# Optimization experiments

Measured on AMD Instinct MI355X. Metric: run time of the kernel, lower is better.

The kernel has to match this reference:

```python
import jax, jax.numpy as jnp
import numpy as np

N_USER = 100000
N_ITEM = 100000
E = 300000
S = 128   # memory / GRU hidden dim (in_feats_s)
T = 128   # time encode dim (in_feats_t)
DE = 128  # edge feature dim
M = 2 * S + T + DE  # GRU input dim (in_feats_m) = 512


def setup_inputs() -> dict:
    key = jax.random.key(0)
    ks = jax.random.split(key, 10)
    si = jax.random.normal(ks[0], (N_USER, S), jnp.float32)
    sj = jax.random.normal(ks[1], (N_ITEM, S), jnp.float32)
    t = jax.random.uniform(ks[2], (E,), jnp.float32)
    e = jax.random.normal(ks[3], (E, DE), jnp.float32)
    src = jax.random.randint(ks[4], (E,), 0, N_USER, jnp.int32)
    dst = jax.random.randint(ks[5], (E,), 0, N_ITEM, jnp.int32)
    # GRU params (torch layout: weight_ih [3H, M], weight_hh [3H, H])
    Wi = jax.random.normal(ks[6], (3 * S, M), jnp.float32) * 0.05
    Wh = jax.random.normal(ks[7], (3 * S, S), jnp.float32) * 0.05
    bi = jax.random.normal(ks[8], (3 * S,), jnp.float32) * 0.05
    bh = jax.random.normal(ks[9], (3 * S,), jnp.float32) * 0.05
    # TimeEncode non-trainable params (phase is zeros, folded out)
    basis_freq = jnp.asarray(1.0 / 10.0 ** np.linspace(0, 9, T), jnp.float32)
    return {"si": si, "sj": sj, "t": t, "e": e, "src": src, "dst": dst,
            "Wi": Wi, "Wh": Wh, "bi": bi, "bh": bh, "basis_freq": basis_freq}


def _last_message(mail, idx, n):
    # DGL last_reduce: message of the highest-edge-id incoming edge per node; zeros if none.
    eid = jnp.arange(mail.shape[0], dtype=jnp.int32)
    last = jax.ops.segment_max(eid, idx, num_segments=n)  # int32 min for empty segments
    has = last >= 0
    safe = jnp.where(has, last, 0)
    return jnp.where(has[:, None], mail[safe], jnp.zeros((), mail.dtype))


def _gru_step(x, h, Wi, Wh, bi, bh):
    gi = x @ Wi.T + bi
    gh = h @ Wh.T + bh
    gir, giz, gin = jnp.split(gi, 3, axis=1)
    ghr, ghz, ghn = jnp.split(gh, 3, axis=1)
    r = jax.nn.sigmoid(gir + ghr)
    z = jax.nn.sigmoid(giz + ghz)
    n = jnp.tanh(gin + r * ghn)
    return (1.0 - z) * n + z * h


def reference(si, sj, t, e, src, dst, Wi, Wh, bi, bh, basis_freq):
    # sinusoidal time encoding (phase = 0)
    te = jnp.cos(t[:, None] * basis_freq[None, :])  # [E, T]
    si_e = si[src]  # [E, S] gather user memory per edge
    sj_e = sj[dst]  # [E, S] gather item memory per edge
    # forward graph g (user->item): mail = [src_mem, dst_mem, time, e], reduce to items
    mail_f = jnp.concatenate([si_e, sj_e, te, e], axis=1)  # [E, M]
    # reverse graph g_r (item->user): src=item, dst=user
    mail_r = jnp.concatenate([sj_e, si_e, te, e], axis=1)  # [E, M]
    mj = _last_message(mail_f, dst, N_ITEM)  # [N_ITEM, M]
    mi = _last_message(mail_r, src, N_USER)  # [N_USER, M]
    si_new = _gru_step(mi, si, Wi, Wh, bi, bh)
    sj_new = _gru_step(mj, sj, Wi, Wh, bi, bh)
    return (si_new, sj_new)
```

## Files before the change

kernel.cpp:

```cpp
#include <hip/hip_runtime.h>
#include <hip/hip_bf16.h>

#define N_USER 100000
#define N_ITEM 100000
#define NE     300000
#define S      128

typedef __attribute__((ext_vector_type(8))) short short8;
typedef __attribute__((ext_vector_type(4))) float floatx4;
typedef unsigned long long ull;

static __device__ __forceinline__ short f2bf(float x) {
  union { float f; unsigned u; } a; a.f = x;
  unsigned r = a.u + 0x7FFFu + ((a.u >> 16) & 1u);
  return (short)(r >> 16);
}

__global__ void prep_kernel(const int* __restrict__ src, const int* __restrict__ dst,
                            int* __restrict__ last_u, int* __restrict__ last_v,
                            const float* __restrict__ Wi, const float* __restrict__ Wh,
                            short* __restrict__ Wp, float* __restrict__ zpage) {
  int b = blockIdx.x;
  int tid = threadIdx.x;
  if (b < 120) {
    int id   = b * 256 + tid;
    int ks   = id / 1536;
    int rem  = id - ks * 1536;
    int lane = rem & 63;
    int col  = (rem >> 6) * 16 + (lane & 15);
    int kof  = (lane >> 4) * 8;
    const float* p = (ks < 16) ? (Wi + (size_t)col * 512 + ks * 32 + kof)
                               : (Wh + (size_t)col * 128 + (ks - 16) * 32 + kof);
    floatx4 a = *(const floatx4*)p;
    floatx4 c = *(const floatx4*)(p + 4);
    short8 v;
    v[0] = f2bf(a[0]); v[1] = f2bf(a[1]); v[2] = f2bf(a[2]); v[3] = f2bf(a[3]);
    v[4] = f2bf(c[0]); v[5] = f2bf(c[1]); v[6] = f2bf(c[2]); v[7] = f2bf(c[3]);
    *(short8*)(Wp + (size_t)id * 8) = v;
  } else if (b == 120) {
    if (tid < 128) zpage[tid] = 0.f;
  } else {
    int i = (b - 121) * 256 + tid;
    if (i < NE) {
      atomicMax(&last_u[src[i]], i);
      atomicMax(&last_v[dst[i]], i);
    }
  }
}

__global__ __launch_bounds__(256, 3)
void fused_gru_kernel(const float* __restrict__ si, const float* __restrict__ sj,
                      const float* __restrict__ tt, const float* __restrict__ ef,
                      const int* __restrict__ src, const int* __restrict__ dst,
                      const float* __restrict__ bi, const float* __restrict__ bh,
                      const float* __restrict__ basis,
                      const int* __restrict__ last_u, const int* __restrict__ last_v,
                      const short* __restrict__ Wp, const float* __restrict__ zpage,
                      float* __restrict__ out) {
  __shared__ short As[20 * 2 * 64 * 8];
  __shared__ ull   Atab[32][5];
  __shared__ float Ttv[32];
  __shared__ float Tsc[32];

  const int tid  = threadIdx.x;
  const int lane = tid & 63;
  const int w    = tid >> 6;
  const int row0 = blockIdx.x * 32;

  if (tid < 32) {
    int g = row0 + tid;
    bool isU = g < N_USER;
    int node = isU ? g : g - N_USER;
    const float* own = (isU ? si : sj) + (size_t)node * S;
    int l = isU ? last_u[node] : last_v[node];
    const float *a0, *a1, *a3; float tv, sc;
    if (l >= 0) {
      int o = isU ? dst[l] : src[l];
      a0 = (isU ? sj : si) + (size_t)o * S;
      a1 = own;
      a3 = ef + (size_t)l * S;
      tv = tt[l]; sc = 1.f;
    } else {
      a0 = zpage; a1 = zpage; a3 = zpage; tv = 0.f; sc = 0.f;
    }
    Atab[tid][0] = (ull)a0; Atab[tid][1] = (ull)a1; Atab[tid][2] = (ull)basis;
    Atab[tid][3] = (ull)a3; Atab[tid][4] = (ull)own;
    Ttv[tid] = tv; Tsc[tid] = sc;
  }
  __syncthreads();

  {
    const int srf = w & 1;
    const int row = srf * 16 + (lane & 15);
    const int kco = (lane >> 4) * 8;
    const int ksb = w >> 1;
    const float tv = Ttv[row], sc = Tsc[row];

    floatx4 va[10], vb[10];
    #pragma unroll
    for (int it = 0; it < 10; ++it) {
      const int seg = it >> 1;
      const int ks  = it * 2 + ksb;
      const int off = ((ks & 3) * 32) + kco;
      const float* p = (const float*)Atab[row][seg] + off;
      va[it] = *(const floatx4*)p;
      vb[it] = *(const floatx4*)(p + 4);
    }
    #pragma unroll
    for (int it = 0; it < 10; ++it) {
      short8 v;
      if (it == 4 || it == 5) {
        v[0] = f2bf(__cosf(tv * va[it][0]) * sc); v[1] = f2bf(__cosf(tv * va[it][1]) * sc);
        v[2] = f2bf(__cosf(tv * va[it][2]) * sc); v[3] = f2bf(__cosf(tv * va[it][3]) * sc);
        v[4] = f2bf(__cosf(tv * vb[it][0]) * sc); v[5] = f2bf(__cosf(tv * vb[it][1]) * sc);
        v[6] = f2bf(__cosf(tv * vb[it][2]) * sc); v[7] = f2bf(__cosf(tv * vb[it][3]) * sc);
      } else {
        v[0] = f2bf(va[it][0]); v[1] = f2bf(va[it][1]);
        v[2] = f2bf(va[it][2]); v[3] = f2bf(va[it][3]);
        v[4] = f2bf(vb[it][0]); v[5] = f2bf(vb[it][1]);
        v[6] = f2bf(vb[it][2]); v[7] = f2bf(vb[it][3]);
      }
      *(short8*)&As[(it * 256 + tid) * 8] = v;
    }
  }
  __syncthreads();

  floatx4 acc[16];
  #pragma unroll
  for (int i = 0; i < 16; ++i) acc[i] = (floatx4){0.f, 0.f, 0.f, 0.f};

  short8 aC[2], bC[6], aN[2], bN[6];
  #pragma unroll
  for (int r2 = 0; r2 < 2; ++r2)
    aC[r2] = *(const short8*)&As[((0 * 2 + r2) * 64 + lane) * 8];
  #pragma unroll
  for (int i = 0; i < 6; ++i)
    bC[i] = *(const short8*)(Wp + (size_t)(((0 * 24) + w + 4 * i) * 64 + lane) * 8);

  #pragma unroll
  for (int ksr = 0; ksr < 20; ++ksr) {
    if (ksr < 19) {
      #pragma unroll
      for (int r2 = 0; r2 < 2; ++r2)
        aN[r2] = *(const short8*)&As[(((ksr + 1) * 2 + r2) * 64 + lane) * 8];
      #pragma unroll
      for (int i = 0; i < 6; ++i)
        bN[i] = *(const short8*)(Wp + (size_t)(((ksr + 1) * 24 + w + 4 * i) * 64 + lane) * 8);
    }
    #pragma unroll
    for (int i = 0; i < 4; ++i)
      #pragma unroll
      for (int r2 = 0; r2 < 2; ++r2)
        acc[i * 2 + r2] = __builtin_amdgcn_mfma_f32_16x16x32_bf16(aC[r2], bC[i], acc[i * 2 + r2], 0, 0, 0);
    if (ksr >= 16) {
      #pragma unroll
      for (int i = 4; i < 6; ++i)
        #pragma unroll
        for (int r2 = 0; r2 < 2; ++r2)
          acc[12 + (i - 4) * 2 + r2] = __builtin_amdgcn_mfma_f32_16x16x32_bf16(aC[r2], bC[i], acc[12 + (i - 4) * 2 + r2], 0, 0, 0);
    } else {
      #pragma unroll
      for (int i = 4; i < 6; ++i)
        #pragma unroll
        for (int r2 = 0; r2 < 2; ++r2)
          acc[i * 2 + r2] = __builtin_amdgcn_mfma_f32_16x16x32_bf16(aC[r2], bC[i], acc[i * 2 + r2], 0, 0, 0);
    }
    #pragma unroll
    for (int r2 = 0; r2 < 2; ++r2) aC[r2] = aN[r2];
    #pragma unroll
    for (int i = 0; i < 6; ++i) bC[i] = bN[i];
  }

  const int colb = lane & 15;
  const int krow = (lane >> 4) * 4;
  #pragma unroll
  for (int h = 0; h < 2; ++h) {
    int c = (w + 4 * h) * 16 + colb;
    float br  = bi[c]       + bh[c];
    float bz  = bi[128 + c] + bh[128 + c];
    float bni = bi[256 + c];
    float bnh = bh[256 + c];
    #pragma unroll
    for (int r2 = 0; r2 < 2; ++r2) {
      #pragma unroll
      for (int k = 0; k < 4; ++k) {
        int row = r2 * 16 + krow + k;
        int g = row0 + row;
        const float* hp = (g < N_USER) ? (si + (size_t)g * S)
                                       : (sj + (size_t)(g - N_USER) * S);
        float rpre = acc[h * 2 + r2][k]       + br;
        float zpre = acc[(2 + h) * 2 + r2][k] + bz;
        float gin  = acc[(4 + h) * 2 + r2][k] + bni;
        float ghn  = acc[12 + h * 2 + r2][k]  + bnh;
        float rg = 1.f / (1.f + __expf(-rpre));
        float zg = 1.f / (1.f + __expf(-zpre));
        float x  = gin + rg * ghn;
        float nn = 1.f - 2.f / (__expf(2.f * x) + 1.f);
        out[(size_t)g * S + c] = (1.f - zg) * nn + zg * hp[c];
      }
    }
  }
}

extern "C" void kernel_launch(void* const* d_in, const int* in_sizes, int n_in,
                              void* d_out, int out_size, void* d_ws, size_t ws_size,
                              hipStream_t stream) {
  const float* si    = (const float*)d_in[0];
  const float* sj    = (const float*)d_in[1];
  const float* tt    = (const float*)d_in[2];
  const float* ef    = (const float*)d_in[3];
  const int*   src   = (const int*)d_in[4];
  const int*   dst   = (const int*)d_in[5];
  const float* Wi    = (const float*)d_in[6];
  const float* Wh    = (const float*)d_in[7];
  const float* bi    = (const float*)d_in[8];
  const float* bh    = (const float*)d_in[9];
  const float* basis = (const float*)d_in[10];

  int*   last_u = (int*)d_ws;
  int*   last_v = last_u + N_USER;
  float* zpage  = (float*)((char*)d_ws + 800000);
  short* Wp     = (short*)((char*)d_ws + (1 << 20));

  hipMemsetAsync(last_u, 0xFF, (size_t)(N_USER + N_ITEM) * sizeof(int), stream);
  prep_kernel<<<121 + (NE + 255) / 256, 256, 0, stream>>>(src, dst, last_u, last_v,
                                                          Wi, Wh, Wp, zpage);
  fused_gru_kernel<<<(N_USER + N_ITEM) / 32, 256, 0, stream>>>(
      si, sj, tt, ef, src, dst, bi, bh, basis, last_u, last_v, Wp, zpage, (float*)d_out);
}
```

Measured before the change: 496.4 us.

## Raise occupancy by trimming registers and dropping the shared pointer table

Raises the launch-bounds occupancy target from 3 to 4 blocks per CU. To reduce register pressure it splits the 10-chunk gather into two halves of 5 and removes the software double-buffering of A/B fragments in the MFMA loop. Each thread now computes its own row's gather pointers directly instead of going through a shared pointer table and a barrier. The cost is that global weight loads are no longer prefetched one k-step ahead, and every thread now does redundant last-index and edge lookups.

```diff
diff --git a/kernel.cpp b/kernel.cpp
--- a/kernel.cpp
+++ b/kernel.cpp
@@ -48,7 +48,7 @@
   }
 }
 
-__global__ __launch_bounds__(256, 3)
+__global__ __launch_bounds__(256, 4)
 void fused_gru_kernel(const float* __restrict__ si, const float* __restrict__ sj,
                       const float* __restrict__ tt, const float* __restrict__ ef,
                       const int* __restrict__ src, const int* __restrict__ dst,
@@ -58,67 +58,62 @@
                       const short* __restrict__ Wp, const float* __restrict__ zpage,
                       float* __restrict__ out) {
   __shared__ short As[20 * 2 * 64 * 8];
-  __shared__ ull   Atab[32][5];
-  __shared__ float Ttv[32];
-  __shared__ float Tsc[32];
 
   const int tid  = threadIdx.x;
   const int lane = tid & 63;
   const int w    = tid >> 6;
   const int row0 = blockIdx.x * 32;
 
-  if (tid < 32) {
-    int g = row0 + tid;
-    bool isU = g < N_USER;
-    int node = isU ? g : g - N_USER;
-    const float* own = (isU ? si : sj) + (size_t)node * S;
-    int l = isU ? last_u[node] : last_v[node];
-    const float *a0, *a1, *a3; float tv, sc;
-    if (l >= 0) {
-      int o = isU ? dst[l] : src[l];
-      a0 = (isU ? sj : si) + (size_t)o * S;
-      a1 = own;
-      a3 = ef + (size_t)l * S;
-      tv = tt[l]; sc = 1.f;
-    } else {
-      a0 = zpage; a1 = zpage; a3 = zpage; tv = 0.f; sc = 0.f;
-    }
-    Atab[tid][0] = (ull)a0; Atab[tid][1] = (ull)a1; Atab[tid][2] = (ull)basis;
-    Atab[tid][3] = (ull)a3; Atab[tid][4] = (ull)own;
-    Ttv[tid] = tv; Tsc[tid] = sc;
-  }
-  __syncthreads();
-
-  {
-    const int srf = w & 1;
-    const int row = srf * 16 + (lane & 15);
-    const int kco = (lane >> 4) * 8;
-    const int ksb = w >> 1;
-    const float tv = Ttv[row], sc = Tsc[row];
-
-    floatx4 va[10], vb[10];
-    #pragma unroll
-    for (int it = 0; it < 10; ++it) {
+  const int srf = w & 1;
+  const int row = srf * 16 + (lane & 15);
+  const int kco = (lane >> 4) * 8;
+  const int ksb = w >> 1;
+
+  const int g0   = row0 + row;
+  const bool isU = g0 < N_USER;
+  const int node = isU ? g0 : g0 - N_USER;
+  const float* own = (isU ? si : sj) + (size_t)node * S;
+  const int l = isU ? last_u[node] : last_v[node];
+  const float* pseg0; const float* pseg1; const float* pseg3;
+  float tv, sc;
+  if (l >= 0) {
+    int o = isU ? dst[l] : src[l];
+    pseg0 = (isU ? sj : si) + (size_t)o * S;
+    pseg1 = own;
+    pseg3 = ef + (size_t)l * S;
+    tv = tt[l]; sc = 1.f;
+  } else {
+    pseg0 = zpage; pseg1 = zpage; pseg3 = zpage; tv = 0.f; sc = 0.f;
+  }
+  const float* pseg[5] = { pseg0, pseg1, basis, pseg3, own };
+
+  #pragma unroll
+  for (int half = 0; half < 2; ++half) {
+    floatx4 va[5], vb[5];
+    #pragma unroll
+    for (int i2 = 0; i2 < 5; ++i2) {
+      const int it  = half * 5 + i2;
       const int seg = it >> 1;
       const int ks  = it * 2 + ksb;
       const int off = ((ks & 3) * 32) + kco;
-      const float* p = (const float*)Atab[row][seg] + off;
-      va[it] = *(const floatx4*)p;
-      vb[it] = *(const floatx4*)(p + 4);
-    }
-    #pragma unroll
-    for (int it = 0; it < 10; ++it) {
+      const float* p = pseg[seg] + off;
+      va[i2] = *(const floatx4*)p;
+      vb[i2] = *(const floatx4*)(p + 4);
+    }
+    #pragma unroll
+    for (int i2 = 0; i2 < 5; ++i2) {
+      const int it = half * 5 + i2;
       short8 v;
       if (it == 4 || it == 5) {
-        v[0] = f2bf(__cosf(tv * va[it][0]) * sc); v[1] = f2bf(__cosf(tv * va[it][1]) * sc);
-        v[2] = f2bf(__cosf(tv * va[it][2]) * sc); v[3] = f2bf(__cosf(tv * va[it][3]) * sc);
-        v[4] = f2bf(__cosf(tv * vb[it][0]) * sc); v[5] = f2bf(__cosf(tv * vb[it][1]) * sc);
-        v[6] = f2bf(__cosf(tv * vb[it][2]) * sc); v[7] = f2bf(__cosf(tv * vb[it][3]) * sc);
+        v[0] = f2bf(__cosf(tv * va[i2][0]) * sc); v[1] = f2bf(__cosf(tv * va[i2][1]) * sc);
+        v[2] = f2bf(__cosf(tv * va[i2][2]) * sc); v[3] = f2bf(__cosf(tv * va[i2][3]) * sc);
+        v[4] = f2bf(__cosf(tv * vb[i2][0]) * sc); v[5] = f2bf(__cosf(tv * vb[i2][1]) * sc);
+        v[6] = f2bf(__cosf(tv * vb[i2][2]) * sc); v[7] = f2bf(__cosf(tv * vb[i2][3]) * sc);
       } else {
-        v[0] = f2bf(va[it][0]); v[1] = f2bf(va[it][1]);
-        v[2] = f2bf(va[it][2]); v[3] = f2bf(va[it][3]);
-        v[4] = f2bf(vb[it][0]); v[5] = f2bf(vb[it][1]);
-        v[6] = f2bf(vb[it][2]); v[7] = f2bf(vb[it][3]);
+        v[0] = f2bf(va[i2][0]); v[1] = f2bf(va[i2][1]);
+        v[2] = f2bf(va[i2][2]); v[3] = f2bf(va[i2][3]);
+        v[4] = f2bf(vb[i2][0]); v[5] = f2bf(vb[i2][1]);
+        v[6] = f2bf(vb[i2][2]); v[7] = f2bf(vb[i2][3]);
       }
       *(short8*)&As[(it * 256 + tid) * 8] = v;
     }
@@ -129,46 +124,32 @@
   #pragma unroll
   for (int i = 0; i < 16; ++i) acc[i] = (floatx4){0.f, 0.f, 0.f, 0.f};
 
-  short8 aC[2], bC[6], aN[2], bN[6];
-  #pragma unroll
-  for (int r2 = 0; r2 < 2; ++r2)
-    aC[r2] = *(const short8*)&As[((0 * 2 + r2) * 64 + lane) * 8];
-  #pragma unroll
-  for (int i = 0; i < 6; ++i)
-    bC[i] = *(const short8*)(Wp + (size_t)(((0 * 24) + w + 4 * i) * 64 + lane) * 8);
-
   #pragma unroll
   for (int ksr = 0; ksr < 20; ++ksr) {
-    if (ksr < 19) {
-      #pragma unroll
-      for (int r2 = 0; r2 < 2; ++r2)
-        aN[r2] = *(const short8*)&As[(((ksr + 1) * 2 + r2) * 64 + lane) * 8];
-      #pragma unroll
-      for (int i = 0; i < 6; ++i)
-        bN[i] = *(const short8*)(Wp + (size_t)(((ksr + 1) * 24 + w + 4 * i) * 64 + lane) * 8);
-    }
-    #pragma unroll
-    for (int i = 0; i < 4; ++i)
-      #pragma unroll
-      for (int r2 = 0; r2 < 2; ++r2)
-        acc[i * 2 + r2] = __builtin_amdgcn_mfma_f32_16x16x32_bf16(aC[r2], bC[i], acc[i * 2 + r2], 0, 0, 0);
+    short8 a0 = *(const short8*)&As[((ksr * 2 + 0) * 64 + lane) * 8];
+    short8 a1 = *(const short8*)&As[((ksr * 2 + 1) * 64 + lane) * 8];
+    short8 b[6];
+    #pragma unroll
+    for (int i = 0; i < 6; ++i)
+      b[i] = *(const short8*)(Wp + (size_t)((ksr * 24 + w + 4 * i) * 64 + lane) * 8);
+    #pragma unroll
+    for (int i = 0; i < 4; ++i) {
+      acc[i * 2 + 0] = __builtin_amdgcn_mfma_f32_16x16x32_bf16(a0, b[i], acc[i * 2 + 0], 0, 0, 0);
+      acc[i * 2 + 1] = __builtin_amdgcn_mfma_f32_16x16x32_bf16(a1, b[i], acc[i * 2 + 1], 0, 0, 0);
+    }
     if (ksr >= 16) {
       #pragma unroll
-      for (int i = 4; i < 6; ++i)
-        #pragma unroll
-        for (int r2 = 0; r2 < 2; ++r2)
-          acc[12 + (i - 4) * 2 + r2] = __builtin_amdgcn_mfma_f32_16x16x32_bf16(aC[r2], bC[i], acc[12 + (i - 4) * 2 + r2], 0, 0, 0);
+      for (int i = 4; i < 6; ++i) {
+        acc[12 + (i - 4) * 2 + 0] = __builtin_amdgcn_mfma_f32_16x16x32_bf16(a0, b[i], acc[12 + (i - 4) * 2 + 0], 0, 0, 0);
+        acc[12 + (i - 4) * 2 + 1] = __builtin_amdgcn_mfma_f32_16x16x32_bf16(a1, b[i], acc[12 + (i - 4) * 2 + 1], 0, 0, 0);
+      }
     } else {
       #pragma unroll
-      for (int i = 4; i < 6; ++i)
-        #pragma unroll
-        for (int r2 = 0; r2 < 2; ++r2)
-          acc[i * 2 + r2] = __builtin_amdgcn_mfma_f32_16x16x32_bf16(aC[r2], bC[i], acc[i * 2 + r2], 0, 0, 0);
-    }
-    #pragma unroll
-    for (int r2 = 0; r2 < 2; ++r2) aC[r2] = aN[r2];
-    #pragma unroll
-    for (int i = 0; i < 6; ++i) bC[i] = bN[i];
+      for (int i = 4; i < 6; ++i) {
+        acc[i * 2 + 0] = __builtin_amdgcn_mfma_f32_16x16x32_bf16(a0, b[i], acc[i * 2 + 0], 0, 0, 0);
+        acc[i * 2 + 1] = __builtin_amdgcn_mfma_f32_16x16x32_bf16(a1, b[i], acc[i * 2 + 1], 0, 0, 0);
+      }
+    }
   }
 
   const int colb = lane & 15;
@@ -184,8 +165,8 @@
     for (int r2 = 0; r2 < 2; ++r2) {
       #pragma unroll
       for (int k = 0; k < 4; ++k) {
-        int row = r2 * 16 + krow + k;
-        int g = row0 + row;
+        int rr = r2 * 16 + krow + k;
+        int g = row0 + rr;
         const float* hp = (g < N_USER) ? (si + (size_t)g * S)
                                        : (sj + (size_t)(g - N_USER) * S);
         float rpre = acc[h * 2 + r2][k]       + br;
```

Result: faster. 484.2 us (-2.5%).
